# Performance work log

Hardware: AMD Instinct MI355X
Metric: run time of the kernel (lower is better)

The kernel has to match this reference:

```python
import jax, jax.numpy as jnp
import numpy as np

N = 50000      # nodes
E = 1_600_000  # edges (avg degree 32)
IN, H, OUT, R = 128, 64, 32, 8
NEG_SLOPE = 0.2


def _rgat(x, src, dst, etype, W, q, k, b, n_nodes):
    """PyG RGATConv, defaults: heads=1, dim=1, additive-self-attention,
    across-relation softmax, concat=True, bias=True, dropout=0 (eval)."""
    # per-relation transform of all nodes: [R, N, O] (cheaper than per-edge bmm since 2*deg >> R)
    t = jnp.einsum('ni,rio->rno', x, W)
    xi = t[etype, dst]                      # [E, O] transformed target feats
    xj = t[etype, src]                      # [E, O] transformed source feats
    a = (xi @ q + xj @ k)[:, 0]             # [E] additive attention logits
    a = jnp.where(a >= 0, a, NEG_SLOPE * a)  # leaky_relu
    # segment softmax over incoming edges of each target node (across relations)
    m = jax.ops.segment_max(a, dst, num_segments=n_nodes)
    m = jnp.where(jnp.isfinite(m), m, 0.0)
    ex = jnp.exp(a - m[dst])
    s = jax.ops.segment_sum(ex, dst, num_segments=n_nodes)
    alpha = ex / (s[dst] + 1e-16)
    out = jax.ops.segment_sum(alpha[:, None] * xj, dst, num_segments=n_nodes)
    return out + b


def setup_inputs() -> dict:
    key = jax.random.key(0)
    ks = jax.random.split(key, 24)
    x = jax.random.normal(ks[0], (N, IN), jnp.float32)
    edge_index = jax.random.randint(ks[1], (2, E), 0, N, jnp.int32)
    edge_type = jax.random.randint(ks[2], (E,), 0, R, jnp.int32)

    def glorot(k, shape, fan_in):
        return jax.random.normal(k, shape, jnp.float32) * (1.0 / np.sqrt(fan_in))

    d = dict(x=x, edge_index=edge_index, edge_type=edge_type)
    # conv1: in->hidden, conv_mu / conv_logvar: hidden->hidden
    d['W1'] = glorot(ks[3], (R, IN, H), IN)
    d['q1'] = glorot(ks[4], (H, 1), H)
    d['k1'] = glorot(ks[5], (H, 1), H)
    d['b1'] = jnp.zeros((H,), jnp.float32)
    d['Wmu'] = glorot(ks[6], (R, H, H), H)
    d['qmu'] = glorot(ks[7], (H, 1), H)
    d['kmu'] = glorot(ks[8], (H, 1), H)
    d['bmu'] = jnp.zeros((H,), jnp.float32)
    d['Wlv'] = glorot(ks[9], (R, H, H), H)
    d['qlv'] = glorot(ks[10], (H, 1), H)
    d['klv'] = glorot(ks[11], (H, 1), H)
    d['blv'] = jnp.zeros((H,), jnp.float32)
    d['Wm'] = glorot(ks[12], (H, OUT), H)   # linear_mu (stored [in,out])
    d['bm'] = jnp.zeros((OUT,), jnp.float32)
    d['Wl'] = glorot(ks[13], (H, OUT), H)   # linear_logvar
    d['bl'] = jnp.zeros((OUT,), jnp.float32)
    return d


def reference(x, edge_index, edge_type, W1, q1, k1, b1,
              Wmu, qmu, kmu, bmu, Wlv, qlv, klv, blv, Wm, bm, Wl, bl):
    src, dst = edge_index[0], edge_index[1]
    hidden = jax.nn.relu(_rgat(x, src, dst, edge_type, W1, q1, k1, b1, N))
    mu = jax.nn.relu(_rgat(hidden, src, dst, edge_type, Wmu, qmu, kmu, bmu, N))
    mu = mu @ Wm + bm                       # dropout is identity in eval
    logvar = jax.nn.relu(_rgat(hidden, src, dst, edge_type, Wlv, qlv, klv, blv, N))
    logvar = logvar @ Wl + bl
    logstd = 0.5 * logvar
    return (mu, logstd)
```

## Files before the change

### kernel.cpp

```cpp
#include <hip/hip_runtime.h>
#include <cstdint>

#define HDIM 64
#define ODIM 32
#define NEG_SLOPE 0.2f
#define SCHUNK 2048

__device__ __forceinline__ unsigned f2bf_rne(float f) {
  unsigned u = __float_as_uint(f);
  return (u + 0x7FFFu + ((u >> 16) & 1u)) >> 16;
}

__global__ __launch_bounds__(256) void count_deg_kernel(
    const int* __restrict__ dst, int* __restrict__ deg, int E) {
  int e = blockIdx.x * 256 + threadIdx.x;
  if (e < E) atomicAdd(&deg[dst[e]], 1);
}

__global__ __launch_bounds__(256) void scan_p1(const int* __restrict__ deg,
                                               int* __restrict__ bsum, int n) {
  int base = blockIdx.x * SCHUNK + threadIdx.x * 8;
  int s = 0;
#pragma unroll
  for (int j = 0; j < 8; j++) {
    int i = base + j;
    if (i < n) s += deg[i];
  }
#pragma unroll
  for (int d = 1; d < 64; d <<= 1) s += __shfl_xor(s, d, 64);
  __shared__ int ws[4];
  if ((threadIdx.x & 63) == 0) ws[threadIdx.x >> 6] = s;
  __syncthreads();
  if (threadIdx.x == 0) bsum[blockIdx.x] = ws[0] + ws[1] + ws[2] + ws[3];
}

__global__ void scan_p2(int* bsum, int nb) {
  int i = threadIdx.x;
  int v = (i < nb) ? bsum[i] : 0;
  int orig = v;
#pragma unroll
  for (int d = 1; d < 64; d <<= 1) {
    int up = __shfl_up(v, d, 64);
    if (i >= d) v += up;
  }
  if (i < nb) bsum[i] = v - orig;
}

__global__ __launch_bounds__(256) void scan_p3(const int* __restrict__ deg,
                                               const int* __restrict__ bsum,
                                               int* __restrict__ row_ptr,
                                               int n) {
  int base = blockIdx.x * SCHUNK + threadIdx.x * 8;
  int vals[8];
  int s = 0;
#pragma unroll
  for (int j = 0; j < 8; j++) {
    int i = base + j;
    vals[j] = (i < n) ? deg[i] : 0;
    s += vals[j];
  }
  int lane = threadIdx.x & 63, w = threadIdx.x >> 6;
  int v = s;
#pragma unroll
  for (int d = 1; d < 64; d <<= 1) {
    int up = __shfl_up(v, d, 64);
    if (lane >= d) v += up;
  }
  __shared__ int wsum[4];
  if (lane == 63) wsum[w] = v;
  __syncthreads();
  int woff = 0;
#pragma unroll
  for (int i = 0; i < 4; i++) woff += (i < w) ? wsum[i] : 0;
  int off = bsum[blockIdx.x] + woff + v - s;
#pragma unroll
  for (int j = 0; j < 8; j++) {
    int i = base + j;
    off += vals[j];
    if (i < n) row_ptr[i + 1] = off;
  }
  if (blockIdx.x == 0 && threadIdx.x == 0) row_ptr[0] = 0;
}

__global__ __launch_bounds__(256) void scatter_kernel(
    const int* __restrict__ src, const int* __restrict__ dst,
    const int* __restrict__ etype, const int* __restrict__ row_ptr,
    int* __restrict__ fill, int* __restrict__ edges, int E) {
  int e = blockIdx.x * 256 + threadIdx.x;
  if (e < E) {
    int d = dst[e];
    int pos = row_ptr[d] + atomicAdd(&fill[d], 1);
    edges[pos] = src[e] | (etype[e] << 16);
  }
}

template <int CIN>
__global__ __launch_bounds__(256) void transform_kernel(
    const float* __restrict__ f, const float* __restrict__ W,
    const float* __restrict__ q, const float* __restrict__ k,
    unsigned short* __restrict__ tb, float* __restrict__ aq,
    float* __restrict__ ak, int N) {
  constexpr int KC = 16;
  constexpr int FLD = 260;
  constexpr int WLD = 68;
  __shared__ float Fl[KC * FLD];
  __shared__ float Wl[KC * WLD];

  const int r = blockIdx.x;
  const int n0 = blockIdx.y * 256;
  const int tid = threadIdx.x;
  const int nt = tid >> 3;
  const int ot = tid & 7;
  const int on0 = ot * 8;

  float acc[8][8];
#pragma unroll
  for (int i = 0; i < 8; i++)
#pragma unroll
    for (int j = 0; j < 8; j++) acc[i][j] = 0.f;

  for (int k0 = 0; k0 < CIN; k0 += KC) {
    {
      const int kk = (tid & 3) * 4;
      const int nb = tid >> 2;
#pragma unroll
      for (int i = 0; i < 4; i++) {
        const int n = nb + i * 64;
        const int gn = n0 + n;
        float4 v = make_float4(0.f, 0.f, 0.f, 0.f);
        if (gn < N) v = *(const float4*)&f[(size_t)gn * CIN + k0 + kk];
        Fl[(kk + 0) * FLD + n] = v.x;
        Fl[(kk + 1) * FLD + n] = v.y;
        Fl[(kk + 2) * FLD + n] = v.z;
        Fl[(kk + 3) * FLD + n] = v.w;
      }
    }
    {
      const int oc = (tid & 15) * 4;
      const int kr = tid >> 4;
      float4 v = *(const float4*)&W[((size_t)r * CIN + k0 + kr) * 64 + oc];
      *(float4*)&Wl[kr * WLD + oc] = v;
    }
    __syncthreads();

#pragma unroll 4
    for (int kk = 0; kk < KC; kk++) {
      float4 fA = *(const float4*)&Fl[kk * FLD + nt * 8];
      float4 fB = *(const float4*)&Fl[kk * FLD + nt * 8 + 4];
      float4 wA = *(const float4*)&Wl[kk * WLD + on0];
      float4 wB = *(const float4*)&Wl[kk * WLD + on0 + 4];
      float fv[8] = {fA.x, fA.y, fA.z, fA.w, fB.x, fB.y, fB.z, fB.w};
      float wv[8] = {wA.x, wA.y, wA.z, wA.w, wB.x, wB.y, wB.z, wB.w};
#pragma unroll
      for (int i = 0; i < 8; i++)
#pragma unroll
        for (int j = 0; j < 8; j++) acc[i][j] = fmaf(fv[i], wv[j], acc[i][j]);
    }
    __syncthreads();
  }

  float qv[8], kv[8];
#pragma unroll
  for (int j = 0; j < 8; j++) {
    qv[j] = q[on0 + j];
    kv[j] = k[on0 + j];
  }

#pragma unroll
  for (int i = 0; i < 8; i++) {
    const int gn = n0 + nt * 8 + i;
    const bool valid = gn < N;
    if (valid) {
      unsigned pk[4];
#pragma unroll
      for (int j = 0; j < 4; j++)
        pk[j] = f2bf_rne(acc[i][2 * j]) | (f2bf_rne(acc[i][2 * j + 1]) << 16);
      *(uint4*)&tb[((size_t)r * N + gn) * 64 + on0] =
          make_uint4(pk[0], pk[1], pk[2], pk[3]);
    }
    float vq = 0.f, vk = 0.f;
#pragma unroll
    for (int j = 0; j < 8; j++) {
      vq = fmaf(acc[i][j], qv[j], vq);
      vk = fmaf(acc[i][j], kv[j], vk);
    }
#pragma unroll
    for (int d = 1; d < 8; d <<= 1) {
      vq += __shfl_xor(vq, d, 64);
      vk += __shfl_xor(vk, d, 64);
    }
    if (ot == 0 && valid) {
      aq[(size_t)r * N + gn] = vq;
      ak[(size_t)r * N + gn] = vk;
    }
  }
}

__global__ __launch_bounds__(256) void transform2_kernel(
    const float* __restrict__ f, const float* __restrict__ Wa,
    const float* __restrict__ Wb, const float* __restrict__ qa,
    const float* __restrict__ ka, const float* __restrict__ qb,
    const float* __restrict__ kb, unsigned* __restrict__ t2p,
    float* __restrict__ aq2, float* __restrict__ ak2, int N) {
  constexpr int CIN = 64, KC = 16;
  constexpr int FLD = 132;
  constexpr int WLD = 68;
  __shared__ float Fl[KC * FLD];
  __shared__ float Wl[2][KC * WLD + 4];

  const int r = blockIdx.x;
  const int n0 = blockIdx.y * 128;
  const int tid = threadIdx.x;
  const int nt = tid >> 4;
  const int ot = tid & 15;
  const int mat = ot >> 3;
  const int on0 = (ot & 7) * 8;

  float acc[8][8];
#pragma unroll
  for (int i = 0; i < 8; i++)
#pragma unroll
    for (int j = 0; j < 8; j++) acc[i][j] = 0.f;

  for (int k0 = 0; k0 < CIN; k0 += KC) {
    {
      const int kk = (tid & 3) * 4;
      const int nb = tid >> 2;
#pragma unroll
      for (int i = 0; i < 2; i++) {
        const int n = nb + i * 64;
        const int gn = n0 + n;
        float4 v = make_float4(0.f, 0.f, 0.f, 0.f);
        if (gn < N) v = *(const float4*)&f[(size_t)gn * CIN + k0 + kk];
        Fl[(kk + 0) * FLD + n] = v.x;
        Fl[(kk + 1) * FLD + n] = v.y;
        Fl[(kk + 2) * FLD + n] = v.z;
        Fl[(kk + 3) * FLD + n] = v.w;
      }
    }
    {
      const int oc = (tid & 15) * 4;
      const int kr = tid >> 4;
      float4 va = *(const float4*)&Wa[((size_t)r * CIN + k0 + kr) * 64 + oc];
      float4 vb = *(const float4*)&Wb[((size_t)r * CIN + k0 + kr) * 64 + oc];
      *(float4*)&Wl[0][kr * WLD + oc] = va;
      *(float4*)&Wl[1][kr * WLD + oc] = vb;
    }
    __syncthreads();

#pragma unroll 4
    for (int kk = 0; kk < KC; kk++) {
      float4 fA = *(const float4*)&Fl[kk * FLD + nt * 8];
      float4 fB = *(const float4*)&Fl[kk * FLD + nt * 8 + 4];
      float4 wA = *(const float4*)&Wl[mat][kk * WLD + on0];
      float4 wB = *(const float4*)&Wl[mat][kk * WLD + on0 + 4];
      float fv[8] = {fA.x, fA.y, fA.z, fA.w, fB.x, fB.y, fB.z, fB.w};
      float wv[8] = {wA.x, wA.y, wA.z, wA.w, wB.x, wB.y, wB.z, wB.w};
#pragma unroll
      for (int i = 0; i < 8; i++)
#pragma unroll
        for (int j = 0; j < 8; j++) acc[i][j] = fmaf(fv[i], wv[j], acc[i][j]);
    }
    __syncthreads();
  }

  const float* qsel = mat ? qb : qa;
  const float* ksel = mat ? kb : ka;
  float qv[8], kv[8];
#pragma unroll
  for (int j = 0; j < 8; j++) {
    qv[j] = qsel[on0 + j];
    kv[j] = ksel[on0 + j];
  }

#pragma unroll
  for (int i = 0; i < 8; i++) {
    const int gn = n0 + nt * 8 + i;
    const bool valid = gn < N;

    unsigned pk[8];
#pragma unroll
    for (int j = 0; j < 8; j++) {
      const float other = __shfl_xor(acc[i][j], 8, 64);
      pk[j] = f2bf_rne(acc[i][j]) | (f2bf_rne(other) << 16);
    }
    if (mat == 0 && valid) {
      unsigned* dst = t2p + ((size_t)r * N + gn) * 64 + on0;
      *(uint4*)dst = make_uint4(pk[0], pk[1], pk[2], pk[3]);
      *(uint4*)(dst + 4) = make_uint4(pk[4], pk[5], pk[6], pk[7]);
    }

    float vq = 0.f, vk = 0.f;
#pragma unroll
    for (int j = 0; j < 8; j++) {
      vq = fmaf(acc[i][j], qv[j], vq);
      vk = fmaf(acc[i][j], kv[j], vk);
    }
#pragma unroll
    for (int d = 1; d < 8; d <<= 1) {
      vq += __shfl_xor(vq, d, 64);
      vk += __shfl_xor(vk, d, 64);
    }
    if ((ot & 7) == 0 && valid) {
      aq2[(size_t)(mat * 8 + r) * N + gn] = vq;
      ak2[(size_t)(mat * 8 + r) * N + gn] = vk;
    }
  }
}

__global__ __launch_bounds__(256) void aggregate_kernel(
    const int* __restrict__ row_ptr, const int* __restrict__ edges,
    const unsigned short* __restrict__ tb, const float* __restrict__ aq,
    const float* __restrict__ ak, const float* __restrict__ bias,
    float* __restrict__ out, int N) {
  const int tid = threadIdx.x;
  const int w = tid >> 6, o = tid & 63;
  int wid = blockIdx.x * 4 + w;
  const bool valid = wid < N;
  if (!valid) wid = N - 1;
  const int beg = row_ptr[wid];
  const int end = valid ? row_ptr[wid + 1] : beg;
  const int deg = end - beg;

  const float aqw = aq[(size_t)(o & 7) * N + wid];

  float m = -1e30f;
  for (int base = 0; base < deg; base += 64) {
    const int j = base + o;
    const int packed = edges[beg + min(j, deg - 1)];
    const int src = packed & 0xFFFF;
    const int rr = packed >> 16;
    float x = __shfl(aqw, rr, 64) + ak[rr * N + src];
    x = (x >= 0.f) ? x : NEG_SLOPE * x;
    m = fmaxf(m, (j < deg) ? x : -1e30f);
  }
#pragma unroll
  for (int d = 1; d < 64; d <<= 1) m = fmaxf(m, __shfl_xor(m, d, 64));

  float s = 0.f, acc = 0.f;
  for (int base = 0; base < deg; base += 64) {
    const int j = base + o;
    const int gcount = min(64, deg - base);
    const int packed = edges[beg + min(j, deg - 1)];
    const int src = packed & 0xFFFF;
    const int rr = packed >> 16;
    const int idx = rr * N + src;
    float x = __shfl(aqw, rr, 64) + ak[idx];
    x = (x >= 0.f) ? x : NEG_SLOPE * x;
    const float p = (j < deg) ? __expf(x - m) : 0.f;
    s += p;
    const int g4 = (gcount + 3) & ~3;
    for (int u = 0; u < g4; u += 4) {
      float pu[4];
      int iu[4];
#pragma unroll
      for (int v = 0; v < 4; v++) {
        pu[v] = __shfl(p, u + v, 64);
        iu[v] = __shfl(idx, u + v, 64);
      }
      unsigned short tv[4];
#pragma unroll
      for (int v = 0; v < 4; v++) tv[v] = tb[(size_t)iu[v] * 64 + o];
#pragma unroll
      for (int v = 0; v < 4; v++)
        acc = fmaf(pu[v], __uint_as_float((unsigned)tv[v] << 16), acc);
    }
  }
#pragma unroll
  for (int d = 1; d < 64; d <<= 1) s += __shfl_xor(s, d, 64);

  if (valid) {
    const float res = acc / (s + 1e-16f) + bias[o];
    out[(size_t)wid * 64 + o] = fmaxf(res, 0.f);
  }
}

__global__ __launch_bounds__(256) void aggregate2_kernel(
    const int* __restrict__ row_ptr, const int* __restrict__ edges,
    const unsigned* __restrict__ t2p, const float* __restrict__ aq2,
    const float* __restrict__ ak2, const float* __restrict__ bmu,
    const float* __restrict__ blv, const float* __restrict__ Wm,
    const float* __restrict__ bm, const float* __restrict__ Wlin,
    const float* __restrict__ bl, float* __restrict__ out_mu,
    float* __restrict__ out_ls, int N) {
  __shared__ float WmL[2048];
  __shared__ float WlL[2048];
  __shared__ float bL[64];
  __shared__ float hL[4][130];
  const int tid = threadIdx.x;
  for (int i = tid; i < 2048; i += 256) {
    WmL[i] = Wm[i];
    WlL[i] = Wlin[i];
  }
  if (tid < 32) {
    bL[tid] = bm[tid];
    bL[32 + tid] = bl[tid];
  }
  __syncthreads();

  const int w = tid >> 6, o = tid & 63;
  int wid = blockIdx.x * 4 + w;
  const bool valid = wid < N;
  if (!valid) wid = N - 1;
  const int beg = row_ptr[wid];
  const int end = valid ? row_ptr[wid + 1] : beg;
  const int deg = end - beg;

  const float aqw = aq2[(size_t)(o & 15) * N + wid];

  float m0 = -1e30f, m1 = -1e30f;
  for (int base = 0; base < deg; base += 64) {
    const int j = base + o;
    const int packed = edges[beg + min(j, deg - 1)];
    const int src = packed & 0xFFFF;
    const int rr = packed >> 16;
    const int idx = rr * N + src;
    float x0 = __shfl(aqw, rr, 64) + ak2[idx];
    float x1 = __shfl(aqw, 8 + rr, 64) + ak2[idx + 8 * N];
    x0 = (x0 >= 0.f) ? x0 : NEG_SLOPE * x0;
    x1 = (x1 >= 0.f) ? x1 : NEG_SLOPE * x1;
    m0 = fmaxf(m0, (j < deg) ? x0 : -1e30f);
    m1 = fmaxf(m1, (j < deg) ? x1 : -1e30f);
  }
#pragma unroll
  for (int d = 1; d < 64; d <<= 1) {
    m0 = fmaxf(m0, __shfl_xor(m0, d, 64));
    m1 = fmaxf(m1, __shfl_xor(m1, d, 64));
  }

  float s0 = 0.f, s1 = 0.f, acc0 = 0.f, acc1 = 0.f;
  for (int base = 0; base < deg; base += 64) {
    const int j = base + o;
    const int gcount = min(64, deg - base);
    const int packed = edges[beg + min(j, deg - 1)];
    const int src = packed & 0xFFFF;
    const int rr = packed >> 16;
    const int idx = rr * N + src;
    float x0 = __shfl(aqw, rr, 64) + ak2[idx];
    float x1 = __shfl(aqw, 8 + rr, 64) + ak2[idx + 8 * N];
    x0 = (x0 >= 0.f) ? x0 : NEG_SLOPE * x0;
    x1 = (x1 >= 0.f) ? x1 : NEG_SLOPE * x1;
    const float p0 = (j < deg) ? __expf(x0 - m0) : 0.f;
    const float p1 = (j < deg) ? __expf(x1 - m1) : 0.f;
    s0 += p0;
    s1 += p1;
    const int g4 = (gcount + 3) & ~3;
    for (int u = 0; u < g4; u += 4) {
      float pu0[4], pu1[4];
      int iu[4];
#pragma unroll
      for (int v = 0; v < 4; v++) {
        pu0[v] = __shfl(p0, u + v, 64);
        pu1[v] = __shfl(p1, u + v, 64);
        iu[v] = __shfl(idx, u + v, 64);
      }
      unsigned pk[4];
#pragma unroll
      for (int v = 0; v < 4; v++) pk[v] = t2p[(size_t)iu[v] * 64 + o];
#pragma unroll
      for (int v = 0; v < 4; v++) {
        acc0 = fmaf(pu0[v], __uint_as_float(pk[v] << 16), acc0);
        acc1 = fmaf(pu1[v], __uint_as_float(pk[v] & 0xFFFF0000u), acc1);
      }
    }
  }
#pragma unroll
  for (int d = 1; d < 64; d <<= 1) {
    s0 += __shfl_xor(s0, d, 64);
    s1 += __shfl_xor(s1, d, 64);
  }

  const float h0 = fmaxf(acc0 / (s0 + 1e-16f) + bmu[o], 0.f);
  const float h1 = fmaxf(acc1 / (s1 + 1e-16f) + blv[o], 0.f);
  hL[w][o] = h0;
  hL[w][64 + o] = h1;
  __syncthreads();

  const float* hrow = &hL[w][(o >= 32) ? 64 : 0];
  const float* WL = (o >= 32) ? WlL : WmL;
  const int j = o & 31;
  float acc = 0.f;
#pragma unroll 8
  for (int c = 0; c < 64; c++) acc = fmaf(hrow[c], WL[c * 32 + j], acc);
  if (valid) {
    if (o < 32)
      out_mu[(size_t)wid * 32 + j] = acc + bL[j];
    else
      out_ls[(size_t)wid * 32 + j] = (acc + bL[32 + j]) * 0.5f;
  }
}

extern "C" void kernel_launch(void* const* d_in, const int* in_sizes, int n_in,
                              void* d_out, int out_size, void* d_ws,
                              size_t ws_size, hipStream_t stream) {
  const float* x = (const float*)d_in[0];
  const int* edge_index = (const int*)d_in[1];
  const int* edge_type = (const int*)d_in[2];
  const float* W1 = (const float*)d_in[3];
  const float* q1 = (const float*)d_in[4];
  const float* k1 = (const float*)d_in[5];
  const float* b1 = (const float*)d_in[6];
  const float* Wmu = (const float*)d_in[7];
  const float* qmu = (const float*)d_in[8];
  const float* kmu = (const float*)d_in[9];
  const float* bmu = (const float*)d_in[10];
  const float* Wlv = (const float*)d_in[11];
  const float* qlv = (const float*)d_in[12];
  const float* klv = (const float*)d_in[13];
  const float* blv = (const float*)d_in[14];
  const float* Wm = (const float*)d_in[15];
  const float* bm = (const float*)d_in[16];
  const float* Wl = (const float*)d_in[17];
  const float* bl = (const float*)d_in[18];

  const int N = in_sizes[0] / 128;
  const int E = in_sizes[2];
  const int R = in_sizes[3] / (128 * 64);

  float* out_mu = (float*)d_out;
  float* out_ls = (float*)d_out + (size_t)N * ODIM;

  char* wsp = (char*)d_ws;
  size_t off = 0;
  auto carve = [&](size_t bytes) {
    void* p = wsp + off;
    off += (bytes + 255) & ~(size_t)255;
    return p;
  };

  void* tbuf = carve((size_t)R * N * 64 * sizeof(unsigned));
  unsigned short* t1b = (unsigned short*)tbuf;
  unsigned* t2p = (unsigned*)tbuf;
  float* aq2 = (float*)carve((size_t)2 * R * N * sizeof(float));
  float* ak2 = (float*)carve((size_t)2 * R * N * sizeof(float));
  float* hidden = (float*)carve((size_t)N * HDIM * sizeof(float));
  int* deg = (int*)carve((size_t)N * sizeof(int));
  int* fill = (int*)carve((size_t)N * sizeof(int));
  int* row_ptr = (int*)carve((size_t)(N + 1) * sizeof(int));
  int* bsum = (int*)carve(256 * sizeof(int));
  int* edges = (int*)carve((size_t)E * sizeof(int));

  const int* e_src = edge_index;
  const int* e_dst = edge_index + E;

  hipMemsetAsync(deg, 0, (size_t)N * sizeof(int), stream);
  hipMemsetAsync(fill, 0, (size_t)N * sizeof(int), stream);
  count_deg_kernel<<<(E + 255) / 256, 256, 0, stream>>>(e_dst, deg, E);
  const int nchunk = (N + SCHUNK - 1) / SCHUNK;
  scan_p1<<<nchunk, 256, 0, stream>>>(deg, bsum, N);
  scan_p2<<<1, 64, 0, stream>>>(bsum, nchunk);
  scan_p3<<<nchunk, 256, 0, stream>>>(deg, bsum, row_ptr, N);
  scatter_kernel<<<(E + 255) / 256, 256, 0, stream>>>(e_src, e_dst, edge_type,
                                                      row_ptr, fill, edges, E);

  const int tiles256 = (N + 255) / 256;
  const int agg_blocks = (N + 3) / 4;

  transform_kernel<128><<<dim3(R, tiles256), 256, 0, stream>>>(
      x, W1, q1, k1, t1b, aq2, ak2, N);
  aggregate_kernel<<<agg_blocks, 256, 0, stream>>>(row_ptr, edges, t1b, aq2,
                                                   ak2, b1, hidden, N);

  const int tiles128 = (N + 127) / 128;
  transform2_kernel<<<dim3(R, tiles128), 256, 0, stream>>>(
      hidden, Wmu, Wlv, qmu, kmu, qlv, klv, t2p, aq2, ak2, N);
  aggregate2_kernel<<<agg_blocks, 256, 0, stream>>>(row_ptr, edges, t2p, aq2,
                                                    ak2, bmu, blv, Wm, bm, Wl,
                                                    bl, out_mu, out_ls, N);
}
```

Baseline: 632.8 us.

## Replace per-node softmax max pass with global per-relation upper bound

```diff
diff --git a/kernel.cpp b/kernel.cpp
--- a/kernel.cpp
+++ b/kernel.cpp
@@ -92,6 +92,20 @@
     int pos = row_ptr[d] + atomicAdd(&fill[d], 1);
     edges[pos] = src[e] | (etype[e] << 16);
   }
+}
+
+__global__ __launch_bounds__(256) void rowmax_kernel(
+    const float* __restrict__ ak, float* __restrict__ maxk, int N) {
+  const float* row = ak + (size_t)blockIdx.x * N;
+  float m = -1e30f;
+  for (int i = threadIdx.x; i < N; i += 256) m = fmaxf(m, row[i]);
+#pragma unroll
+  for (int d = 1; d < 64; d <<= 1) m = fmaxf(m, __shfl_xor(m, d, 64));
+  __shared__ float ws[4];
+  if ((threadIdx.x & 63) == 0) ws[threadIdx.x >> 6] = m;
+  __syncthreads();
+  if (threadIdx.x == 0)
+    maxk[blockIdx.x] = fmaxf(fmaxf(ws[0], ws[1]), fmaxf(ws[2], ws[3]));
 }
 
 template <int CIN>
@@ -311,8 +325,8 @@
 __global__ __launch_bounds__(256) void aggregate_kernel(
     const int* __restrict__ row_ptr, const int* __restrict__ edges,
     const unsigned short* __restrict__ tb, const float* __restrict__ aq,
-    const float* __restrict__ ak, const float* __restrict__ bias,
-    float* __restrict__ out, int N) {
+    const float* __restrict__ ak, const float* __restrict__ maxk,
+    const float* __restrict__ bias, float* __restrict__ out, int N) {
   const int tid = threadIdx.x;
   const int w = tid >> 6, o = tid & 63;
   int wid = blockIdx.x * 4 + w;
@@ -324,18 +338,11 @@
 
   const float aqw = aq[(size_t)(o & 7) * N + wid];
 
-  float m = -1e30f;
-  for (int base = 0; base < deg; base += 64) {
-    const int j = base + o;
-    const int packed = edges[beg + min(j, deg - 1)];
-    const int src = packed & 0xFFFF;
-    const int rr = packed >> 16;
-    float x = __shfl(aqw, rr, 64) + ak[rr * N + src];
-    x = (x >= 0.f) ? x : NEG_SLOPE * x;
-    m = fmaxf(m, (j < deg) ? x : -1e30f);
-  }
-#pragma unroll
-  for (int d = 1; d < 64; d <<= 1) m = fmaxf(m, __shfl_xor(m, d, 64));
+  float v = aqw + maxk[o & 7];
+  v = (v >= 0.f) ? v : NEG_SLOPE * v;
+#pragma unroll
+  for (int d = 1; d < 8; d <<= 1) v = fmaxf(v, __shfl_xor(v, d, 64));
+  const float m = __shfl(v, 0, 64);
 
   float s = 0.f, acc = 0.f;
   for (int base = 0; base < deg; base += 64) {
@@ -349,21 +356,21 @@
     x = (x >= 0.f) ? x : NEG_SLOPE * x;
     const float p = (j < deg) ? __expf(x - m) : 0.f;
     s += p;
-    const int g4 = (gcount + 3) & ~3;
-    for (int u = 0; u < g4; u += 4) {
-      float pu[4];
-      int iu[4];
-#pragma unroll
-      for (int v = 0; v < 4; v++) {
-        pu[v] = __shfl(p, u + v, 64);
-        iu[v] = __shfl(idx, u + v, 64);
+    const int g8 = (gcount + 7) & ~7;
+    for (int u = 0; u < g8; u += 8) {
+      float pu[8];
+      int iu[8];
+#pragma unroll
+      for (int q = 0; q < 8; q++) {
+        pu[q] = __shfl(p, u + q, 64);
+        iu[q] = __shfl(idx, u + q, 64);
       }
-      unsigned short tv[4];
-#pragma unroll
-      for (int v = 0; v < 4; v++) tv[v] = tb[(size_t)iu[v] * 64 + o];
-#pragma unroll
-      for (int v = 0; v < 4; v++)
-        acc = fmaf(pu[v], __uint_as_float((unsigned)tv[v] << 16), acc);
+      unsigned short tv[8];
+#pragma unroll
+      for (int q = 0; q < 8; q++) tv[q] = tb[(size_t)iu[q] * 64 + o];
+#pragma unroll
+      for (int q = 0; q < 8; q++)
+        acc = fmaf(pu[q], __uint_as_float((unsigned)tv[q] << 16), acc);
     }
   }
 #pragma unroll
@@ -378,11 +385,11 @@
 __global__ __launch_bounds__(256) void aggregate2_kernel(
     const int* __restrict__ row_ptr, const int* __restrict__ edges,
     const unsigned* __restrict__ t2p, const float* __restrict__ aq2,
-    const float* __restrict__ ak2, const float* __restrict__ bmu,
-    const float* __restrict__ blv, const float* __restrict__ Wm,
-    const float* __restrict__ bm, const float* __restrict__ Wlin,
-    const float* __restrict__ bl, float* __restrict__ out_mu,
-    float* __restrict__ out_ls, int N) {
+    const float* __restrict__ ak2, const float* __restrict__ maxk2,
+    const float* __restrict__ bmu, const float* __restrict__ blv,
+    const float* __restrict__ Wm, const float* __restrict__ bm,
+    const float* __restrict__ Wlin, const float* __restrict__ bl,
+    float* __restrict__ out_mu, float* __restrict__ out_ls, int N) {
   __shared__ float WmL[2048];
   __shared__ float WlL[2048];
   __shared__ float bL[64];
@@ -408,25 +415,12 @@
 
   const float aqw = aq2[(size_t)(o & 15) * N + wid];
 
-  float m0 = -1e30f, m1 = -1e30f;
-  for (int base = 0; base < deg; base += 64) {
-    const int j = base + o;
-    const int packed = edges[beg + min(j, deg - 1)];
-    const int src = packed & 0xFFFF;
-    const int rr = packed >> 16;
-    const int idx = rr * N + src;
-    float x0 = __shfl(aqw, rr, 64) + ak2[idx];
-    float x1 = __shfl(aqw, 8 + rr, 64) + ak2[idx + 8 * N];
-    x0 = (x0 >= 0.f) ? x0 : NEG_SLOPE * x0;
-    x1 = (x1 >= 0.f) ? x1 : NEG_SLOPE * x1;
-    m0 = fmaxf(m0, (j < deg) ? x0 : -1e30f);
-    m1 = fmaxf(m1, (j < deg) ? x1 : -1e30f);
-  }
-#pragma unroll
-  for (int d = 1; d < 64; d <<= 1) {
-    m0 = fmaxf(m0, __shfl_xor(m0, d, 64));
-    m1 = fmaxf(m1, __shfl_xor(m1, d, 64));
-  }
+  float v = aqw + maxk2[o & 15];
+  v = (v >= 0.f) ? v : NEG_SLOPE * v;
+#pragma unroll
+  for (int d = 1; d < 8; d <<= 1) v = fmaxf(v, __shfl_xor(v, d, 64));
+  const float m0 = __shfl(v, 0, 64);
+  const float m1 = __shfl(v, 8, 64);
 
   float s0 = 0.f, s1 = 0.f, acc0 = 0.f, acc1 = 0.f;
   for (int base = 0; base < deg; base += 64) {
@@ -444,23 +438,23 @@
     const float p1 = (j < deg) ? __expf(x1 - m1) : 0.f;
     s0 += p0;
     s1 += p1;
-    const int g4 = (gcount + 3) & ~3;
-    for (int u = 0; u < g4; u += 4) {
-      float pu0[4], pu1[4];
-      int iu[4];
-#pragma unroll
-      for (int v = 0; v < 4; v++) {
-        pu0[v] = __shfl(p0, u + v, 64);
-        pu1[v] = __shfl(p1, u + v, 64);
-        iu[v] = __shfl(idx, u + v, 64);
+    const int g8 = (gcount + 7) & ~7;
+    for (int u = 0; u < g8; u += 8) {
+      float pu0[8], pu1[8];
+      int iu[8];
+#pragma unroll
+      for (int q = 0; q < 8; q++) {
+        pu0[q] = __shfl(p0, u + q, 64);
+        pu1[q] = __shfl(p1, u + q, 64);
+        iu[q] = __shfl(idx, u + q, 64);
       }
-      unsigned pk[4];
-#pragma unroll
-      for (int v = 0; v < 4; v++) pk[v] = t2p[(size_t)iu[v] * 64 + o];
-#pragma unroll
-      for (int v = 0; v < 4; v++) {
-        acc0 = fmaf(pu0[v], __uint_as_float(pk[v] << 16), acc0);
-        acc1 = fmaf(pu1[v], __uint_as_float(pk[v] & 0xFFFF0000u), acc1);
+      unsigned pk[8];
+#pragma unroll
+      for (int q = 0; q < 8; q++) pk[q] = t2p[(size_t)iu[q] * 64 + o];
+#pragma unroll
+      for (int q = 0; q < 8; q++) {
+        acc0 = fmaf(pu0[q], __uint_as_float(pk[q] << 16), acc0);
+        acc1 = fmaf(pu1[q], __uint_as_float(pk[q] & 0xFFFF0000u), acc1);
       }
     }
   }
@@ -534,6 +528,7 @@
   float* aq2 = (float*)carve((size_t)2 * R * N * sizeof(float));
   float* ak2 = (float*)carve((size_t)2 * R * N * sizeof(float));
   float* hidden = (float*)carve((size_t)N * HDIM * sizeof(float));
+  float* maxk = (float*)carve(2 * R * sizeof(float));
   int* deg = (int*)carve((size_t)N * sizeof(int));
   int* fill = (int*)carve((size_t)N * sizeof(int));
   int* row_ptr = (int*)carve((size_t)(N + 1) * sizeof(int));
@@ -558,13 +553,15 @@
 
   transform_kernel<128><<<dim3(R, tiles256), 256, 0, stream>>>(
       x, W1, q1, k1, t1b, aq2, ak2, N);
-  aggregate_kernel<<<agg_blocks, 256, 0, stream>>>(row_ptr, edges, t1b, aq2,
-                                                   ak2, b1, hidden, N);
+  rowmax_kernel<<<R, 256, 0, stream>>>(ak2, maxk, N);
+  aggregate_kernel<<<agg_blocks, 256, 0, stream>>>(
+      row_ptr, edges, t1b, aq2, ak2, maxk, b1, hidden, N);
 
   const int tiles128 = (N + 127) / 128;
   transform2_kernel<<<dim3(R, tiles128), 256, 0, stream>>>(
       hidden, Wmu, Wlv, qmu, kmu, qlv, klv, t2p, aq2, ak2, N);
-  aggregate2_kernel<<<agg_blocks, 256, 0, stream>>>(row_ptr, edges, t2p, aq2,
-                                                    ak2, bmu, blv, Wm, bm, Wl,
-                                                    bl, out_mu, out_ls, N);
-}
+  rowmax_kernel<<<2 * R, 256, 0, stream>>>(ak2, maxk, N);
+  aggregate2_kernel<<<agg_blocks, 256, 0, stream>>>(
+      row_ptr, edges, t2p, aq2, ak2, maxk, bmu, blv, Wm, bm, Wl, bl, out_mu,
+      out_ls, N);
+}
```

New measurement: 690.1 us. +9.1%, slower.
